# Performance work log

Measured on AMD Instinct MI355X. Metric: run time of the kernel, lower is better.

The kernel has to match this reference:

```python
import jax, jax.numpy as jnp
import numpy as np

GROUP_SIZE = 128  # K-rows sharing one dequant scale


def _dequant(B, s):
    """Unpack int4 (uint4b8: value = nibble - 8) from packed int32 and apply group scales.
    B: [K//8, N] int32, 8 nibbles per word along K (nibble i -> k = 8*row + i).
    s: [K//GROUP_SIZE, N] float scales.
    Returns W: [K, N] float.
    """
    Kp, N = B.shape
    K = Kp * 8
    shifts = (jnp.arange(8, dtype=jnp.int32) * 4)
    # [Kp, 8, N] nibbles -> [K, N]
    nib = (B[:, None, :] >> shifts[None, :, None]) & 0xF
    w = nib.reshape(K, N).astype(s.dtype) - 8.0
    # per-group scaling: groups of GROUP_SIZE consecutive K rows
    w = (w.reshape(K // GROUP_SIZE, GROUP_SIZE, N) * s[:, None, :]).reshape(K, N)
    return w


def setup_inputs() -> dict:
    key = jax.random.key(0)
    k1, k2, k3 = jax.random.split(key, 3)
    M, K, N = 64, 8192, 8192
    x = jax.random.normal(k1, (M, K), dtype=jnp.float32)
    B = jax.random.randint(k2, (K // 8, N), 0, 2147483647, dtype=jnp.int32)
    s = jax.random.uniform(k3, (K // GROUP_SIZE, N), dtype=jnp.float32) * 0.02
    return {"x": x, "B": B, "s": s}


def reference(x, B, s):
    # machete_mm: fused int4 dequant + GEMM; here expressed as dequant then matmul
    w = _dequant(B, s)          # [K, N]
    out = x @ w                 # [M, N]
    return out
```

## Files before the change

### kernel.cpp

```cpp
#include <hip/hip_runtime.h>

typedef _Float16 half2v __attribute__((ext_vector_type(2)));
typedef _Float16 half8  __attribute__((ext_vector_type(8)));
typedef float    floatx4 __attribute__((ext_vector_type(4)));

#define M_DIM 64
#define K_DIM 8192
#define N_DIM 8192
#define NT 512
#define KSB 16

__global__ __launch_bounds__(256) void permute_x_kernel(
        const float* __restrict__ x, _Float16* __restrict__ xp) {
    const int t  = blockIdx.x * 256 + threadIdx.x;
    const int c  = t & 15;
    const int q  = (t >> 4) & 3;
    const int mt = (t >> 6) & 3;
    const int kb = t >> 8;
    const int m  = mt * 16 + c;
    const int k0 = kb * 32 + q * 8;
    const float* src = x + (size_t)m * K_DIM + k0;
    float4 a = *(const float4*)(src);
    float4 b = *(const float4*)(src + 4);
    union { _Float16 h[8]; float4 f; } u;
    u.h[0] = (_Float16)a.x; u.h[1] = (_Float16)b.x;
    u.h[2] = (_Float16)a.y; u.h[3] = (_Float16)b.y;
    u.h[4] = (_Float16)a.z; u.h[5] = (_Float16)b.z;
    u.h[6] = (_Float16)a.w; u.h[7] = (_Float16)b.w;
    *(float4*)(xp + (size_t)t * 8) = u.f;
}

__device__ __forceinline__ void dma16(const void* g, void* l) {
    __builtin_amdgcn_global_load_lds(
        (const __attribute__((address_space(1))) unsigned int*)(uintptr_t)g,
        (__attribute__((address_space(3))) unsigned int*)(uintptr_t)l,
        16, 0, 0);
}

__device__ __forceinline__ half2v dq_pair(unsigned int bits, half2v sub, half2v sc) {
    union { unsigned int u; half2v h; } cv;
    cv.u = bits;
    return (cv.h - sub) * sc;
}

__global__ __launch_bounds__(1024, 4) void machete_mm_kernel(
        const _Float16* __restrict__ xp,
        const unsigned int* __restrict__ Bq,
        const float* __restrict__ s,
        _Float16* __restrict__ partial) {
    __shared__ char astage[2][16384];

    const int tid  = threadIdx.x;
    const int w    = tid >> 6;
    const int lane = tid & 63;
    const int c    = lane & 15;
    const int q    = lane >> 4;
    const int ns   = blockIdx.x;
    const int kb   = blockIdx.y;
    const int wc   = ns * NT + w * 32;

    half2v s2[4][2];
    #pragma unroll
    for (int g = 0; g < 4; ++g) {
        const float f0 = s[(size_t)(kb * 4 + g) * N_DIM + wc + c];
        const float f1 = s[(size_t)(kb * 4 + g) * N_DIM + wc + 16 + c];
        s2[g][0] = (half2v){ (_Float16)f0, (_Float16)f0 };
        s2[g][1] = (half2v){ (_Float16)f1, (_Float16)f1 };
    }
    const half2v c1032 = { (_Float16)1032.0f, (_Float16)1032.0f };

    const char* a_base = (const char*)xp + (size_t)kb * 65536;
    const unsigned int* b_base = Bq + (size_t)(kb * 64) * N_DIM + wc + c;

    auto bload = [&](int st, int d, int t) {
        return b_base[(size_t)(st * 16 + d * 4 + q) * N_DIM + 16 * t];
    };
    auto stage_dma = [&](int st, int p) {
        dma16(a_base + (size_t)st * 16384 + w * 1024 + lane * 16,
              &astage[p][w * 1024]);
    };

    floatx4 acc[4][2];
    #pragma unroll
    for (int i = 0; i < 4; ++i) { acc[i][0] = (floatx4)0.0f; acc[i][1] = (floatx4)0.0f; }

    unsigned int bcur[2][4], bnxt[2][4];
    #pragma unroll
    for (int d = 0; d < 4; ++d) { bcur[0][d] = bload(0, d, 0); bcur[1][d] = bload(0, d, 1); }
    stage_dma(0, 0);
    __syncthreads();

    #pragma unroll
    for (int st = 0; st < 4; ++st) {
        const int p = st & 1;
        if (st < 3) {
            #pragma unroll
            for (int d = 0; d < 4; ++d) {
                bnxt[0][d] = bload(st + 1, d, 0);
                bnxt[1][d] = bload(st + 1, d, 1);
            }
            stage_dma(st + 1, p ^ 1);
        }

        #pragma unroll
        for (int d = 0; d < 4; ++d) {
            half8 afr[4];
            #pragma unroll
            for (int mt = 0; mt < 4; ++mt)
                afr[mt] = *(const half8*)(&astage[p][(d * 4 + mt) * 1024 + lane * 16]);
            #pragma unroll
            for (int t = 0; t < 2; ++t) {
                const unsigned int wd = bcur[t][d];
                const half2v sc = s2[st][t];
                union { half2v h2[4]; half8 h8; } b8;
                b8.h2[0] = dq_pair(( wd        & 0x000F000Fu) | 0x64006400u, c1032, sc);
                b8.h2[1] = dq_pair(((wd >> 4)  & 0x000F000Fu) | 0x64006400u, c1032, sc);
                b8.h2[2] = dq_pair(((wd >> 8)  & 0x000F000Fu) | 0x64006400u, c1032, sc);
                b8.h2[3] = dq_pair(((wd >> 12) & 0x000F000Fu) | 0x64006400u, c1032, sc);
                #pragma unroll
                for (int mt = 0; mt < 4; ++mt)
                    acc[mt][t] = __builtin_amdgcn_mfma_f32_16x16x32_f16(
                        afr[mt], b8.h8, acc[mt][t], 0, 0, 0);
            }
        }
        __syncthreads();
        #pragma unroll
        for (int d = 0; d < 4; ++d) { bcur[0][d] = bnxt[0][d]; bcur[1][d] = bnxt[1][d]; }
    }

    _Float16* pt = partial + (size_t)(kb * M_DIM) * N_DIM;
    #pragma unroll
    for (int mt = 0; mt < 4; ++mt)
        #pragma unroll
        for (int t = 0; t < 2; ++t)
            #pragma unroll
            for (int r = 0; r < 4; ++r) {
                const int m = mt * 16 + q * 4 + r;
                pt[(size_t)m * N_DIM + wc + 16 * t + c] = (_Float16)acc[mt][t][r];
            }
}

__global__ __launch_bounds__(256) void reduce_kernel(
        const _Float16* __restrict__ partial, float* __restrict__ out) {
    const size_t i = ((size_t)blockIdx.x * 256 + threadIdx.x) * 8;
    const size_t S = (size_t)M_DIM * N_DIM;
    float a[8] = {0, 0, 0, 0, 0, 0, 0, 0};
    #pragma unroll
    for (int bk = 0; bk < KSB; ++bk) {
        const half8 hv = *(const half8*)(partial + bk * S + i);
        #pragma unroll
        for (int j = 0; j < 8; ++j) a[j] += (float)hv[j];
    }
    float4 v0 = { a[0], a[1], a[2], a[3] };
    float4 v1 = { a[4], a[5], a[6], a[7] };
    *(float4*)(out + i)     = v0;
    *(float4*)(out + i + 4) = v1;
}

extern "C" void kernel_launch(void* const* d_in, const int* in_sizes, int n_in,
                              void* d_out, int out_size, void* d_ws, size_t ws_size,
                              hipStream_t stream) {
    const float*        x  = (const float*)d_in[0];
    const unsigned int* Bq = (const unsigned int*)d_in[1];
    const float*        sc = (const float*)d_in[2];
    float* out        = (float*)d_out;
    _Float16* xp      = (_Float16*)d_ws;
    _Float16* partial = (_Float16*)((char*)d_ws + (1 << 20));

    permute_x_kernel<<<dim3(M_DIM * K_DIM / 8 / 256), 256, 0, stream>>>(x, xp);
    machete_mm_kernel<<<dim3(N_DIM / NT, KSB), 1024, 0, stream>>>(xp, Bq, sc, partial);
    reduce_kernel<<<dim3(M_DIM * N_DIM / (256 * 8)), 256, 0, stream>>>(partial, out);
}
```

Measured before the change: 95.12 us.

## Replace split-K partial buffer and reduce kernel with in-block LDS reduction plus atomics

Each 1024-thread block now covers a 128-column N tile and a 2048-deep K slice. Its four groups of four waves each handle a quarter of that slice, so the split-K factor across blocks drops from 16 to 4. Partial accumulators are combined through a two-step tree reduction in LDS, and the final values are atomically added into the fp32 output, which the permute kernel now zeroes. This removes the fp16 partial-sum round trip through global memory and the separate reduce launch. In exchange it adds global float atomics and grows the LDS staging buffer to 128 KB per block, which limits residency to one block per CU.

```diff
diff --git a/kernel.cpp b/kernel.cpp
--- a/kernel.cpp
+++ b/kernel.cpp
@@ -7,11 +7,12 @@
 #define M_DIM 64
 #define K_DIM 8192
 #define N_DIM 8192
-#define NT 512
-#define KSB 16
+#define NT 128
+#define KSB 4
 
 __global__ __launch_bounds__(256) void permute_x_kernel(
-        const float* __restrict__ x, _Float16* __restrict__ xp) {
+        const float* __restrict__ x, _Float16* __restrict__ xp,
+        float* __restrict__ out) {
     const int t  = blockIdx.x * 256 + threadIdx.x;
     const int c  = t & 15;
     const int q  = (t >> 4) & 3;
@@ -28,6 +29,10 @@
     u.h[4] = (_Float16)a.z; u.h[5] = (_Float16)b.z;
     u.h[6] = (_Float16)a.w; u.h[7] = (_Float16)b.w;
     *(float4*)(xp + (size_t)t * 8) = u.f;
+    const float4 z = {0.f, 0.f, 0.f, 0.f};
+    float* o = out + (size_t)t * 8;
+    *(float4*)(o)     = z;
+    *(float4*)(o + 4) = z;
 }
 
 __device__ __forceinline__ void dma16(const void* g, void* l) {
@@ -47,37 +52,43 @@
         const _Float16* __restrict__ xp,
         const unsigned int* __restrict__ Bq,
         const float* __restrict__ s,
-        _Float16* __restrict__ partial) {
-    __shared__ char astage[2][16384];
+        float* __restrict__ out) {
+    __shared__ char astage[2][65536];
 
     const int tid  = threadIdx.x;
     const int w    = tid >> 6;
     const int lane = tid & 63;
     const int c    = lane & 15;
     const int q    = lane >> 4;
+    const int cw   = w & 3;
+    const int ks   = w >> 2;
     const int ns   = blockIdx.x;
     const int kb   = blockIdx.y;
-    const int wc   = ns * NT + w * 32;
+    const int wc   = ns * NT + cw * 32;
 
     half2v s2[4][2];
     #pragma unroll
     for (int g = 0; g < 4; ++g) {
-        const float f0 = s[(size_t)(kb * 4 + g) * N_DIM + wc + c];
-        const float f1 = s[(size_t)(kb * 4 + g) * N_DIM + wc + 16 + c];
+        const size_t row = (size_t)(kb * 16 + ks * 4 + g) * N_DIM;
+        const float f0 = s[row + wc + c];
+        const float f1 = s[row + wc + 16 + c];
         s2[g][0] = (half2v){ (_Float16)f0, (_Float16)f0 };
         s2[g][1] = (half2v){ (_Float16)f1, (_Float16)f1 };
     }
     const half2v c1032 = { (_Float16)1032.0f, (_Float16)1032.0f };
 
-    const char* a_base = (const char*)xp + (size_t)kb * 65536;
-    const unsigned int* b_base = Bq + (size_t)(kb * 64) * N_DIM + wc + c;
+    const char* a_base = (const char*)xp + (size_t)(kb * 64 + ks * 16) * 4096;
+    const unsigned int* b_base = Bq + (size_t)(kb * 256 + ks * 64) * N_DIM + wc + c;
 
-    auto bload = [&](int st, int d, int t) {
-        return b_base[(size_t)(st * 16 + d * 4 + q) * N_DIM + 16 * t];
+    auto bload = [&](int r, int d, int t) {
+        return b_base[(size_t)(r * 16 + d * 4 + q) * N_DIM + 16 * t];
     };
-    auto stage_dma = [&](int st, int p) {
-        dma16(a_base + (size_t)st * 16384 + w * 1024 + lane * 16,
-              &astage[p][w * 1024]);
+    auto stage_dma = [&](int r, int p) {
+        const char* src = a_base + (size_t)(r * 4 + cw) * 4096 + lane * 16;
+        char* dst = &astage[p][ks * 16384 + cw * 4096];
+        #pragma unroll
+        for (int i = 0; i < 4; ++i)
+            dma16(src + i * 1024, dst + i * 1024);
     };
 
     floatx4 acc[4][2];
@@ -91,15 +102,15 @@
     __syncthreads();
 
     #pragma unroll
-    for (int st = 0; st < 4; ++st) {
-        const int p = st & 1;
-        if (st < 3) {
+    for (int r = 0; r < 4; ++r) {
+        const int p = r & 1;
+        if (r < 3) {
             #pragma unroll
             for (int d = 0; d < 4; ++d) {
-                bnxt[0][d] = bload(st + 1, d, 0);
-                bnxt[1][d] = bload(st + 1, d, 1);
+                bnxt[0][d] = bload(r + 1, d, 0);
+                bnxt[1][d] = bload(r + 1, d, 1);
             }
-            stage_dma(st + 1, p ^ 1);
+            stage_dma(r + 1, p ^ 1);
         }
 
         #pragma unroll
@@ -107,11 +118,12 @@
             half8 afr[4];
             #pragma unroll
             for (int mt = 0; mt < 4; ++mt)
-                afr[mt] = *(const half8*)(&astage[p][(d * 4 + mt) * 1024 + lane * 16]);
+                afr[mt] = *(const half8*)(
+                    &astage[p][ks * 16384 + (d * 4 + mt) * 1024 + lane * 16]);
             #pragma unroll
             for (int t = 0; t < 2; ++t) {
                 const unsigned int wd = bcur[t][d];
-                const half2v sc = s2[st][t];
+                const half2v sc = s2[r][t];
                 union { half2v h2[4]; half8 h8; } b8;
                 b8.h2[0] = dq_pair(( wd        & 0x000F000Fu) | 0x64006400u, c1032, sc);
                 b8.h2[1] = dq_pair(((wd >> 4)  & 0x000F000Fu) | 0x64006400u, c1032, sc);
@@ -128,33 +140,46 @@
         for (int d = 0; d < 4; ++d) { bcur[0][d] = bnxt[0][d]; bcur[1][d] = bnxt[1][d]; }
     }
 
-    _Float16* pt = partial + (size_t)(kb * M_DIM) * N_DIM;
-    #pragma unroll
-    for (int mt = 0; mt < 4; ++mt)
+    float* red = (float*)astage;
+    auto spill = [&](int slot) {
+        float* b = red + (size_t)slot * 2048 + lane;
         #pragma unroll
-        for (int t = 0; t < 2; ++t)
+        for (int mt = 0; mt < 4; ++mt)
             #pragma unroll
-            for (int r = 0; r < 4; ++r) {
-                const int m = mt * 16 + q * 4 + r;
-                pt[(size_t)m * N_DIM + wc + 16 * t + c] = (_Float16)acc[mt][t][r];
-            }
-}
-
-__global__ __launch_bounds__(256) void reduce_kernel(
-        const _Float16* __restrict__ partial, float* __restrict__ out) {
-    const size_t i = ((size_t)blockIdx.x * 256 + threadIdx.x) * 8;
-    const size_t S = (size_t)M_DIM * N_DIM;
-    float a[8] = {0, 0, 0, 0, 0, 0, 0, 0};
-    #pragma unroll
-    for (int bk = 0; bk < KSB; ++bk) {
-        const half8 hv = *(const half8*)(partial + bk * S + i);
+            for (int t = 0; t < 2; ++t)
+                #pragma unroll
+                for (int rr = 0; rr < 4; ++rr)
+                    b[(mt * 8 + t * 4 + rr) * 64] = acc[mt][t][rr];
+    };
+    auto gather = [&](int slot) {
+        const float* b = red + (size_t)slot * 2048 + lane;
         #pragma unroll
-        for (int j = 0; j < 8; ++j) a[j] += (float)hv[j];
+        for (int mt = 0; mt < 4; ++mt)
+            #pragma unroll
+            for (int t = 0; t < 2; ++t)
+                #pragma unroll
+                for (int rr = 0; rr < 4; ++rr)
+                    acc[mt][t][rr] += b[(mt * 8 + t * 4 + rr) * 64];
+    };
+    if (ks >= 2) spill(w - 8);
+    __syncthreads();
+    if (ks < 2) gather(w);
+    __syncthreads();
+    if (ks == 1) spill(w - 4);
+    __syncthreads();
+    if (ks == 0) {
+        gather(w);
+        #pragma unroll
+        for (int mt = 0; mt < 4; ++mt)
+            #pragma unroll
+            for (int t = 0; t < 2; ++t)
+                #pragma unroll
+                for (int rr = 0; rr < 4; ++rr) {
+                    const int m = mt * 16 + q * 4 + rr;
+                    unsafeAtomicAdd(out + (size_t)m * N_DIM + wc + 16 * t + c,
+                                    acc[mt][t][rr]);
+                }
     }
-    float4 v0 = { a[0], a[1], a[2], a[3] };
-    float4 v1 = { a[4], a[5], a[6], a[7] };
-    *(float4*)(out + i)     = v0;
-    *(float4*)(out + i + 4) = v1;
 }
 
 extern "C" void kernel_launch(void* const* d_in, const int* in_sizes, int n_in,
@@ -163,11 +188,9 @@
     const float*        x  = (const float*)d_in[0];
     const unsigned int* Bq = (const unsigned int*)d_in[1];
     const float*        sc = (const float*)d_in[2];
-    float* out        = (float*)d_out;
-    _Float16* xp      = (_Float16*)d_ws;
-    _Float16* partial = (_Float16*)((char*)d_ws + (1 << 20));
+    float* out   = (float*)d_out;
+    _Float16* xp = (_Float16*)d_ws;
 
-    permute_x_kernel<<<dim3(M_DIM * K_DIM / 8 / 256), 256, 0, stream>>>(x, xp);
-    machete_mm_kernel<<<dim3(N_DIM / NT, KSB), 1024, 0, stream>>>(xp, Bq, sc, partial);
-    reduce_kernel<<<dim3(M_DIM * N_DIM / (256 * 8)), 256, 0, stream>>>(partial, out);
+    permute_x_kernel<<<dim3(M_DIM * K_DIM / 8 / 256), 256, 0, stream>>>(x, xp, out);
+    machete_mm_kernel<<<dim3(N_DIM / NT, KSB), 1024, 0, stream>>>(xp, Bq, sc, out);
 }
```

New measurement: 94.04 us. About the same (-1.1%).
